# Performance work log

Measured on AMD Instinct MI355X. Metric: run time of the kernel, lower is better.

The kernel has to match this reference:

```python
import jax, jax.numpy as jnp
import numpy as np

NUM_CHANNELS = 64
IN_FEATURES = 256
OUT_FEATURES = 256
B = 128
N = 2048


def setup_inputs() -> dict:
    key = jax.random.key(0)
    k_x, k_c, k_w, k_b = jax.random.split(key, 4)
    x = jax.random.normal(k_x, (B, N, IN_FEATURES), dtype=jnp.float32)
    channels = jax.random.randint(k_c, (N,), 0, NUM_CHANNELS, dtype=jnp.int64)
    # kaiming_uniform_(a=sqrt(5)) over fan_in -> bound = 1/sqrt(fan_in)
    wb = 1.0 / np.sqrt(IN_FEATURES)
    weight = jax.random.uniform(k_w, (NUM_CHANNELS, OUT_FEATURES, IN_FEATURES),
                                dtype=jnp.float32, minval=-wb, maxval=wb)
    bias = jax.random.uniform(k_b, (NUM_CHANNELS, OUT_FEATURES),
                              dtype=jnp.float32, minval=-wb, maxval=wb)
    return {"x": x, "channels": channels, "weight": weight, "bias": bias}


def reference(x, channels, weight, bias):
    # Gather per-point weights/biases by channel id (shared across batch).
    w = weight[channels]          # [N, out, in]
    b = bias[channels]            # [N, out]
    # Equivalent to bmm over the point axis: [B,N,in] x [N,out,in] -> [B,N,out]
    y = jnp.einsum('bni,noi->bno', x, w)
    y = y + b                     # broadcast over batch
    y = jnp.tanh(y)               # activation=True
    y = y + x                     # residual mode 1 (out == in)
    return (y, channels)
```

## Files before the change

### kernel.cpp

```cpp
#include <hip/hip_runtime.h>
#include <hip/hip_bf16.h>


#define N_SZ 2048

typedef __attribute__((ext_vector_type(8))) __bf16 bf16x8;
typedef __attribute__((ext_vector_type(4))) float  f32x4;

__device__ __forceinline__ unsigned f2bf1(float f) {
    union { float f; unsigned u; } v; v.f = f;
    return (v.u + 0x7fffu + ((v.u >> 16) & 1u)) >> 16;
}
__device__ __forceinline__ int pack2(float lo, float hi) {
    return (int)(f2bf1(lo) | (f2bf1(hi) << 16));
}
__device__ __forceinline__ float bf2f(unsigned u16) {
    union { unsigned u; float f; } v; v.u = u16 << 16;
    return v.f;
}
__device__ __forceinline__ float tanh_fast(float s) {
    float a = fabsf(s);
    float t = __expf(-2.0f * a);
    float r = (1.0f - t) * __builtin_amdgcn_rcpf(1.0f + t);
    return __builtin_copysignf(r, s);
}

__global__ __launch_bounds__(1024) void sort_kernel(const int* __restrict__ channels,
                                                    int* __restrict__ perm,
                                                    int* __restrict__ start,
                                                    float* __restrict__ out_ch) {
    __shared__ int cnt[64], off[64];
    const int t = threadIdx.x;
    if (t < 64) cnt[t] = 0;
    __syncthreads();
    const int n0 = t, n1 = t + 1024;
    const int c0 = channels[n0], c1 = channels[n1];
    atomicAdd(&cnt[c0], 1);
    atomicAdd(&cnt[c1], 1);
    out_ch[n0] = (float)c0;
    out_ch[n1] = (float)c1;
    __syncthreads();
    if (t == 0) {
        int s = 0;
        for (int i = 0; i < 64; ++i) { start[i] = s; off[i] = s; s += cnt[i]; }
        start[64] = s;
    }
    __syncthreads();
    int p0 = atomicAdd(&off[c0], 1); perm[p0] = n0;
    int p1 = atomicAdd(&off[c1], 1); perm[p1] = n1;
}

__global__ __launch_bounds__(256) void wconv_kernel(const float* __restrict__ w,
                                                    unsigned short* __restrict__ wsW) {
    const size_t t = (size_t)blockIdx.x * 256 + threadIdx.x;
    const float* src = w + t * 8;
    float4 f0 = *(const float4*)(src);
    float4 f1 = *(const float4*)(src + 4);
    int4 p;
    p.x = pack2(f0.x, f0.y); p.y = pack2(f0.z, f0.w);
    p.z = pack2(f1.x, f1.y); p.w = pack2(f1.z, f1.w);
    *(int4*)(wsW + t * 8) = p;
}

__global__ __launch_bounds__(512, 2) void channel_dense_kernel(
    const float* __restrict__ x, const int* __restrict__ perm,
    const int* __restrict__ start, const unsigned short* __restrict__ wsW,
    const float* __restrict__ bias, float* __restrict__ y)
{
    __shared__ __align__(16) unsigned char sA[2][65536];

    const int c = blockIdx.x >> 2, chunk = blockIdx.x & 3;
    const int s0 = start[c], cnt = start[c + 1] - s0;
    const int p_begin = s0 + ((cnt * chunk) >> 2);
    const int p_end   = s0 + ((cnt * (chunk + 1)) >> 2);
    if (p_begin >= p_end) return;

    const int tid  = threadIdx.x;
    const int lane = tid & 63, wv = tid >> 6;
    const int lr   = lane & 15, lg4 = lane >> 4;

    bf16x8 wreg[2][8];
    {
        const unsigned short* wb = wsW + ((size_t)c << 16);
        #pragma unroll
        for (int mo = 0; mo < 2; ++mo) {
            const unsigned short* wr_ = wb + (wv * 32 + mo * 16 + lr) * 256 + lg4 * 8;
            #pragma unroll
            for (int kt = 0; kt < 8; ++kt)
                wreg[mo][kt] = *(const bf16x8*)(wr_ + kt * 32);
        }
    }
    float4 bv[2];
    bv[0] = *(const float4*)(bias + c * 256 + wv * 32 + lg4 * 4);
    bv[1] = *(const float4*)(bias + c * 256 + wv * 32 + 16 + lg4 * 4);

    const int r  = tid >> 2;
    const int qt = tid & 3;
    const int wbyte = (r * 64 + qt * 16) ^ ((r & 7) << 4);
    float4 la[8];

    auto stage_load = [&](int n_, int h) {
        const float* xb = x + ((size_t)r * N_SZ + n_) * 256 + h * 128 + qt * 8;
        #pragma unroll
        for (int j = 0; j < 4; ++j) {
            la[2 * j]     = *(const float4*)(xb + j * 32);
            la[2 * j + 1] = *(const float4*)(xb + j * 32 + 4);
        }
    };
    auto stage_write = [&](int buf, int h) {
        #pragma unroll
        for (int j = 0; j < 4; ++j) {
            int4 p;
            p.x = pack2(la[2*j].x,   la[2*j].y);   p.y = pack2(la[2*j].z,   la[2*j].w);
            p.z = pack2(la[2*j+1].x, la[2*j+1].y); p.w = pack2(la[2*j+1].z, la[2*j+1].w);
            *(int4*)(&sA[buf][(h * 4 + j) * 8192 + wbyte]) = p;
        }
    };

    int n_cur = perm[p_begin];
    int n_nxt = 0;

    stage_load(n_cur, 0); stage_write(0, 0);
    stage_load(n_cur, 1); stage_write(0, 1);
    __syncthreads();

    const int lanebyte = (lr * 64 + lg4 * 16) ^ ((lr & 7) << 4);

    for (int p = p_begin; p < p_end; ++p) {
        const int cur = (p - p_begin) & 1, nxt = cur ^ 1;
        const bool more = (p + 1 < p_end);
        if (more) { n_nxt = perm[p + 1]; stage_load(n_nxt, 0); }

        f32x4 acc[2][8] = {};
        #pragma unroll
        for (int kt = 0; kt < 8; ++kt) {
            bf16x8 xf[8];
            #pragma unroll
            for (int nb = 0; nb < 8; ++nb)
                xf[nb] = *(const bf16x8*)(&sA[cur][kt * 8192 + nb * 1024 + lanebyte]);
            #pragma unroll
            for (int nb = 0; nb < 8; ++nb) {
                acc[0][nb] = __builtin_amdgcn_mfma_f32_16x16x32_bf16(wreg[0][kt], xf[nb], acc[0][nb], 0, 0, 0);
                acc[1][nb] = __builtin_amdgcn_mfma_f32_16x16x32_bf16(wreg[1][kt], xf[nb], acc[1][nb], 0, 0, 0);
            }
        }

        if (more) { stage_write(nxt, 0); stage_load(n_nxt, 1); }

        #pragma unroll
        for (int mo = 0; mo < 2; ++mo) {
            const int o0 = wv * 32 + mo * 16 + lg4 * 4;
            #pragma unroll
            for (int nb = 0; nb < 8; ++nb) {
                const int b = nb * 16 + lr;
                uint2 rv = *(const uint2*)(&sA[cur][wv * 8192 +
                              ((b * 64 + mo * 32 + lg4 * 8) ^ ((lr & 7) << 4))]);
                float4 o;
                o.x = tanh_fast(acc[mo][nb][0] + bv[mo].x) + bf2f(rv.x & 0xffffu);
                o.y = tanh_fast(acc[mo][nb][1] + bv[mo].y) + bf2f(rv.x >> 16);
                o.z = tanh_fast(acc[mo][nb][2] + bv[mo].z) + bf2f(rv.y & 0xffffu);
                o.w = tanh_fast(acc[mo][nb][3] + bv[mo].w) + bf2f(rv.y >> 16);
                *(float4*)(y + ((size_t)b * N_SZ + n_cur) * 256 + o0) = o;
            }
        }

        if (more) stage_write(nxt, 1);
        __syncthreads();
        n_cur = n_nxt;
    }
}

extern "C" void kernel_launch(void* const* d_in, const int* in_sizes, int n_in,
                              void* d_out, int out_size, void* d_ws, size_t ws_size,
                              hipStream_t stream) {
    const float* x        = (const float*)d_in[0];
    const int*   channels = (const int*)d_in[1];
    const float* weight   = (const float*)d_in[2];
    const float* bias     = (const float*)d_in[3];
    float* y = (float*)d_out;

    unsigned short* wsW = (unsigned short*)d_ws;
    int* perm  = (int*)((unsigned char*)d_ws + (64u << 17));
    int* start = perm + 2048;

    sort_kernel<<<dim3(1), dim3(1024), 0, stream>>>(
        channels, perm, start, y + (size_t)128 * N_SZ * 256);
    wconv_kernel<<<dim3(2048), dim3(256), 0, stream>>>(weight, wsW);
    channel_dense_kernel<<<dim3(256), dim3(512), 0, stream>>>(
        x, perm, start, wsW, bias, y);
}
```

Measured before the change: 220.6 us.

## Launch one block per point-half instead of per-channel persistent loop

Replaces the per-channel persistent blocks (256 blocks looping over sorted points with double-buffered LDS) with 4096 short-lived blocks, each handling one point and half of the batch. The channel id is packed into the perm entries so no start table is needed, and blocks are ordered in a strided pattern so neighbouring blocks come from different channel runs. Weights are now streamed from global/L2 each kernel iteration instead of being held in registers. LDS per block drops to 32KB, allowing higher occupancy, which is meant to fix load imbalance and exposed memory latency. The trade-off is repeated weight loads and the loss of explicit prefetch overlap.

```diff
diff --git a/kernel.cpp b/kernel.cpp
--- a/kernel.cpp
+++ b/kernel.cpp
@@ -7,13 +7,6 @@
 typedef __attribute__((ext_vector_type(8))) __bf16 bf16x8;
 typedef __attribute__((ext_vector_type(4))) float  f32x4;
 
-__device__ __forceinline__ unsigned f2bf1(float f) {
-    union { float f; unsigned u; } v; v.f = f;
-    return (v.u + 0x7fffu + ((v.u >> 16) & 1u)) >> 16;
-}
-__device__ __forceinline__ int pack2(float lo, float hi) {
-    return (int)(f2bf1(lo) | (f2bf1(hi) << 16));
-}
 __device__ __forceinline__ float bf2f(unsigned u16) {
     union { unsigned u; float f; } v; v.u = u16 << 16;
     return v.f;
@@ -24,10 +17,15 @@
     float r = (1.0f - t) * __builtin_amdgcn_rcpf(1.0f + t);
     return __builtin_copysignf(r, s);
 }
+__device__ __forceinline__ bf16x8 cvt8(float4 a, float4 b) {
+    bf16x8 v;
+    v[0] = (__bf16)a.x; v[1] = (__bf16)a.y; v[2] = (__bf16)a.z; v[3] = (__bf16)a.w;
+    v[4] = (__bf16)b.x; v[5] = (__bf16)b.y; v[6] = (__bf16)b.z; v[7] = (__bf16)b.w;
+    return v;
+}
 
 __global__ __launch_bounds__(1024) void sort_kernel(const int* __restrict__ channels,
                                                     int* __restrict__ perm,
-                                                    int* __restrict__ start,
                                                     float* __restrict__ out_ch) {
     __shared__ int cnt[64], off[64];
     const int t = threadIdx.x;
@@ -40,14 +38,10 @@
     out_ch[n0] = (float)c0;
     out_ch[n1] = (float)c1;
     __syncthreads();
-    if (t == 0) {
-        int s = 0;
-        for (int i = 0; i < 64; ++i) { start[i] = s; off[i] = s; s += cnt[i]; }
-        start[64] = s;
-    }
+    if (t == 0) { int s = 0; for (int i = 0; i < 64; ++i) { off[i] = s; s += cnt[i]; } }
     __syncthreads();
-    int p0 = atomicAdd(&off[c0], 1); perm[p0] = n0;
-    int p1 = atomicAdd(&off[c1], 1); perm[p1] = n1;
+    int p0 = atomicAdd(&off[c0], 1); perm[p0] = n0 | (c0 << 16);
+    int p1 = atomicAdd(&off[c1], 1); perm[p1] = n1 | (c1 << 16);
 }
 
 __global__ __launch_bounds__(256) void wconv_kernel(const float* __restrict__ w,
@@ -56,117 +50,81 @@
     const float* src = w + t * 8;
     float4 f0 = *(const float4*)(src);
     float4 f1 = *(const float4*)(src + 4);
-    int4 p;
-    p.x = pack2(f0.x, f0.y); p.y = pack2(f0.z, f0.w);
-    p.z = pack2(f1.x, f1.y); p.w = pack2(f1.z, f1.w);
-    *(int4*)(wsW + t * 8) = p;
+    bf16x8 v = cvt8(f0, f1);
+    *(bf16x8*)(wsW + t * 8) = v;
 }
 
-__global__ __launch_bounds__(512, 2) void channel_dense_kernel(
+__global__ __launch_bounds__(512, 4) void channel_dense_kernel(
     const float* __restrict__ x, const int* __restrict__ perm,
-    const int* __restrict__ start, const unsigned short* __restrict__ wsW,
-    const float* __restrict__ bias, float* __restrict__ y)
+    const unsigned short* __restrict__ wsW, const float* __restrict__ bias,
+    float* __restrict__ y)
 {
-    __shared__ __align__(16) unsigned char sA[2][65536];
+    __shared__ __align__(16) unsigned char sA[32768];
 
-    const int c = blockIdx.x >> 2, chunk = blockIdx.x & 3;
-    const int s0 = start[c], cnt = start[c + 1] - s0;
-    const int p_begin = s0 + ((cnt * chunk) >> 2);
-    const int p_end   = s0 + ((cnt * (chunk + 1)) >> 2);
-    if (p_begin >= p_end) return;
+    const int g    = blockIdx.x;
+    const int lg   = (g & 7) * 512 + (g >> 3);
+    const int pv   = perm[lg >> 1];
+    const int n    = pv & 0xffff;
+    const int c    = pv >> 16;
+    const int half = lg & 1;
+    const int tid  = threadIdx.x;
 
-    const int tid  = threadIdx.x;
+    {
+        const int r = tid >> 3;
+        const int q = tid & 7;
+        const float* xr = x + ((size_t)(half * 64 + r) * N_SZ + n) * 256 + q * 32;
+        float4 la[8];
+        #pragma unroll
+        for (int j = 0; j < 8; ++j) la[j] = *(const float4*)(xr + j * 4);
+        const int swz = (r & 7) << 4;
+        #pragma unroll
+        for (int j = 0; j < 4; ++j) {
+            bf16x8 v = cvt8(la[2 * j], la[2 * j + 1]);
+            *(bf16x8*)(sA + q * 4096 + ((r * 64 + j * 16) ^ swz)) = v;
+        }
+    }
+    __syncthreads();
+
     const int lane = tid & 63, wv = tid >> 6;
     const int lr   = lane & 15, lg4 = lane >> 4;
 
-    bf16x8 wreg[2][8];
-    {
-        const unsigned short* wb = wsW + ((size_t)c << 16);
+    const unsigned short* wl = wsW + (((size_t)c * 256 + wv * 32 + lr) << 8) + lg4 * 8;
+    const int lanebyte = (lr * 64 + lg4 * 16) ^ ((lr & 7) << 4);
+
+    f32x4 acc[2][4] = {};
+
+    #pragma unroll
+    for (int kt = 0; kt < 8; ++kt) {
+        bf16x8 wf0 = *(const bf16x8*)(wl + kt * 32);
+        bf16x8 wf1 = *(const bf16x8*)(wl + 16 * 256 + kt * 32);
+        bf16x8 xf[4];
         #pragma unroll
-        for (int mo = 0; mo < 2; ++mo) {
-            const unsigned short* wr_ = wb + (wv * 32 + mo * 16 + lr) * 256 + lg4 * 8;
-            #pragma unroll
-            for (int kt = 0; kt < 8; ++kt)
-                wreg[mo][kt] = *(const bf16x8*)(wr_ + kt * 32);
+        for (int nb = 0; nb < 4; ++nb)
+            xf[nb] = *(const bf16x8*)(sA + kt * 4096 + nb * 1024 + lanebyte);
+        #pragma unroll
+        for (int nb = 0; nb < 4; ++nb) {
+            acc[0][nb] = __builtin_amdgcn_mfma_f32_16x16x32_bf16(wf0, xf[nb], acc[0][nb], 0, 0, 0);
+            acc[1][nb] = __builtin_amdgcn_mfma_f32_16x16x32_bf16(wf1, xf[nb], acc[1][nb], 0, 0, 0);
         }
     }
-    float4 bv[2];
-    bv[0] = *(const float4*)(bias + c * 256 + wv * 32 + lg4 * 4);
-    bv[1] = *(const float4*)(bias + c * 256 + wv * 32 + 16 + lg4 * 4);
 
-    const int r  = tid >> 2;
-    const int qt = tid & 3;
-    const int wbyte = (r * 64 + qt * 16) ^ ((r & 7) << 4);
-    float4 la[8];
-
-    auto stage_load = [&](int n_, int h) {
-        const float* xb = x + ((size_t)r * N_SZ + n_) * 256 + h * 128 + qt * 8;
+    #pragma unroll
+    for (int mo = 0; mo < 2; ++mo) {
+        const int o0 = wv * 32 + mo * 16 + lg4 * 4;
+        const float4 bv = *(const float4*)(bias + c * 256 + o0);
         #pragma unroll
-        for (int j = 0; j < 4; ++j) {
-            la[2 * j]     = *(const float4*)(xb + j * 32);
-            la[2 * j + 1] = *(const float4*)(xb + j * 32 + 4);
+        for (int nb = 0; nb < 4; ++nb) {
+            const int rl = nb * 16 + lr;
+            const int b  = half * 64 + rl;
+            const int rbyte = wv * 4096 + ((rl * 64 + mo * 32 + lg4 * 8) ^ ((rl & 7) << 4));
+            uint2 rv = *(const uint2*)(sA + rbyte);
+            float4 o;
+            o.x = tanh_fast(acc[mo][nb][0] + bv.x) + bf2f(rv.x & 0xffffu);
+            o.y = tanh_fast(acc[mo][nb][1] + bv.y) + bf2f(rv.x >> 16);
+            o.z = tanh_fast(acc[mo][nb][2] + bv.z) + bf2f(rv.y & 0xffffu);
+            o.w = tanh_fast(acc[mo][nb][3] + bv.w) + bf2f(rv.y >> 16);
+            *(float4*)(y + ((size_t)b * N_SZ + n) * 256 + o0) = o;
         }
-    };
-    auto stage_write = [&](int buf, int h) {
-        #pragma unroll
-        for (int j = 0; j < 4; ++j) {
-            int4 p;
-            p.x = pack2(la[2*j].x,   la[2*j].y);   p.y = pack2(la[2*j].z,   la[2*j].w);
-            p.z = pack2(la[2*j+1].x, la[2*j+1].y); p.w = pack2(la[2*j+1].z, la[2*j+1].w);
-            *(int4*)(&sA[buf][(h * 4 + j) * 8192 + wbyte]) = p;
-        }
-    };
-
-    int n_cur = perm[p_begin];
-    int n_nxt = 0;
-
-    stage_load(n_cur, 0); stage_write(0, 0);
-    stage_load(n_cur, 1); stage_write(0, 1);
-    __syncthreads();
-
-    const int lanebyte = (lr * 64 + lg4 * 16) ^ ((lr & 7) << 4);
-
-    for (int p = p_begin; p < p_end; ++p) {
-        const int cur = (p - p_begin) & 1, nxt = cur ^ 1;
-        const bool more = (p + 1 < p_end);
-        if (more) { n_nxt = perm[p + 1]; stage_load(n_nxt, 0); }
-
-        f32x4 acc[2][8] = {};
-        #pragma unroll
-        for (int kt = 0; kt < 8; ++kt) {
-            bf16x8 xf[8];
-            #pragma unroll
-            for (int nb = 0; nb < 8; ++nb)
-                xf[nb] = *(const bf16x8*)(&sA[cur][kt * 8192 + nb * 1024 + lanebyte]);
-            #pragma unroll
-            for (int nb = 0; nb < 8; ++nb) {
-                acc[0][nb] = __builtin_amdgcn_mfma_f32_16x16x32_bf16(wreg[0][kt], xf[nb], acc[0][nb], 0, 0, 0);
-                acc[1][nb] = __builtin_amdgcn_mfma_f32_16x16x32_bf16(wreg[1][kt], xf[nb], acc[1][nb], 0, 0, 0);
-            }
-        }
-
-        if (more) { stage_write(nxt, 0); stage_load(n_nxt, 1); }
-
-        #pragma unroll
-        for (int mo = 0; mo < 2; ++mo) {
-            const int o0 = wv * 32 + mo * 16 + lg4 * 4;
-            #pragma unroll
-            for (int nb = 0; nb < 8; ++nb) {
-                const int b = nb * 16 + lr;
-                uint2 rv = *(const uint2*)(&sA[cur][wv * 8192 +
-                              ((b * 64 + mo * 32 + lg4 * 8) ^ ((lr & 7) << 4))]);
-                float4 o;
-                o.x = tanh_fast(acc[mo][nb][0] + bv[mo].x) + bf2f(rv.x & 0xffffu);
-                o.y = tanh_fast(acc[mo][nb][1] + bv[mo].y) + bf2f(rv.x >> 16);
-                o.z = tanh_fast(acc[mo][nb][2] + bv[mo].z) + bf2f(rv.y & 0xffffu);
-                o.w = tanh_fast(acc[mo][nb][3] + bv[mo].w) + bf2f(rv.y >> 16);
-                *(float4*)(y + ((size_t)b * N_SZ + n_cur) * 256 + o0) = o;
-            }
-        }
-
-        if (more) stage_write(nxt, 1);
-        __syncthreads();
-        n_cur = n_nxt;
     }
 }
 
@@ -180,12 +138,11 @@
     float* y = (float*)d_out;
 
     unsigned short* wsW = (unsigned short*)d_ws;
-    int* perm  = (int*)((unsigned char*)d_ws + (64u << 17));
-    int* start = perm + 2048;
+    int* perm = (int*)((unsigned char*)d_ws + (64u << 17));
 
     sort_kernel<<<dim3(1), dim3(1024), 0, stream>>>(
-        channels, perm, start, y + (size_t)128 * N_SZ * 256);
+        channels, perm, y + (size_t)128 * N_SZ * 256);
     wconv_kernel<<<dim3(2048), dim3(256), 0, stream>>>(weight, wsW);
-    channel_dense_kernel<<<dim3(256), dim3(512), 0, stream>>>(
-        x, perm, start, wsW, bias, y);
+    channel_dense_kernel<<<dim3(4096), dim3(512), 0, stream>>>(
+        x, perm, wsW, bias, y);
 }
```

Measured after the change: 190.7 us. 13.6% less time.
